# Kernel optimization log

Measured on AMD Instinct MI355X. Metric: run time of the kernel, lower is better.

The kernel has to match this reference:

```python
import jax, jax.numpy as jnp
import numpy as np
from jax import lax

N, H, W, T = 8, 100, 152, 256
STRIDE = 8
ANCHOR_SIZE = 64.0
PRE_NMS_THRESH = 0.05
PRE_NMS_TOP_N = 1000
NMS_THRESH = 0.6
POST_TOP_N = 100
IMG_H, IMG_W = 800, 1216
BW = (10.0, 10.0, 5.0, 5.0)          # BoxCoder weights (wx, wy, ww, wh)
DWH_CLIP = float(np.log(1000.0 / 16.0))
TO_REMOVE = 1.0


def setup_inputs() -> dict:
    key = jax.random.key(0)
    k1, k2, k3 = jax.random.split(key, 3)
    box_regression = jax.random.normal(k1, (N, 4, H, W), dtype=jnp.float32)
    centerness = jax.random.normal(k2, (N, 1, H, W), dtype=jnp.float32)
    dot_product_logits = jax.random.normal(k3, (N, H * W, T), dtype=jnp.float32)
    # anchor grid matching permute_and_flatten's (H, W, A) row-major ordering
    ys, xs = jnp.meshgrid(jnp.arange(H, dtype=jnp.float32),
                          jnp.arange(W, dtype=jnp.float32), indexing="ij")
    cx = xs.reshape(-1) * STRIDE + STRIDE / 2.0
    cy = ys.reshape(-1) * STRIDE + STRIDE / 2.0
    half = ANCHOR_SIZE / 2.0
    anc = jnp.stack([cx - half, cy - half, cx + half, cy + half], axis=-1)  # [H*W, 4]
    anchors = jnp.broadcast_to(anc, (N, H * W, 4)).astype(jnp.float32)
    return {"box_regression": box_regression, "centerness": centerness,
            "anchors": anchors, "dot_product_logits": dot_product_logits}


def _decode(rel, anc):
    w = anc[..., 2] - anc[..., 0] + TO_REMOVE
    h = anc[..., 3] - anc[..., 1] + TO_REMOVE
    cx = anc[..., 0] + 0.5 * w
    cy = anc[..., 1] + 0.5 * h
    dx = rel[..., 0] / BW[0]
    dy = rel[..., 1] / BW[1]
    dw = jnp.minimum(rel[..., 2] / BW[2], DWH_CLIP)
    dh = jnp.minimum(rel[..., 3] / BW[3], DWH_CLIP)
    pcx = dx * w + cx
    pcy = dy * h + cy
    pw = jnp.exp(dw) * w
    ph = jnp.exp(dh) * h
    return jnp.stack([pcx - 0.5 * pw, pcy - 0.5 * ph,
                      pcx + 0.5 * pw - 1.0, pcy + 0.5 * ph - 1.0], axis=-1)


def _iou_one_vs_all(box, boxes):
    area1 = (box[2] - box[0] + TO_REMOVE) * (box[3] - box[1] + TO_REMOVE)
    area2 = (boxes[:, 2] - boxes[:, 0] + TO_REMOVE) * (boxes[:, 3] - boxes[:, 1] + TO_REMOVE)
    lt = jnp.maximum(box[:2], boxes[:, :2])
    rb = jnp.minimum(box[2:], boxes[:, 2:])
    wh = jnp.maximum(rb - lt + TO_REMOVE, 0.0)
    inter = wh[:, 0] * wh[:, 1]
    return inter / (area1 + area2 - inter)


def _nms_single(boxes, scores):
    # greedy NMS, fixed POST_TOP_N iterations (fpn_post_nms_top_n)
    def step(s, _):
        j = jnp.argmax(s)
        sj = s[j]
        bj = boxes[j]
        flag = (sj > 0).astype(boxes.dtype)
        ious = _iou_one_vs_all(bj, boxes)
        s = jnp.where(ious > NMS_THRESH, 0.0, s).at[j].set(0.0)
        return s, (bj * flag, sj * flag)
    _, (kb, ks) = lax.scan(step, scores, None, length=POST_TOP_N)
    return kb, ks


def reference(box_regression, centerness, anchors, dot_product_logits):
    n, _, h, w = box_regression.shape
    # sigmoid + MEAN token aggregation  -> [N, HWA]
    scores = jax.nn.sigmoid(dot_product_logits).mean(-1)
    # permute_and_flatten: [N,4A,H,W] -> [N, HWA, 4]
    box_reg = box_regression.reshape(n, 1, 4, h, w).transpose(0, 3, 4, 1, 2).reshape(n, -1, 4)
    ctr = jax.nn.sigmoid(centerness.reshape(n, 1, 1, h, w).transpose(0, 3, 4, 1, 2).reshape(n, -1))
    cand = scores > PRE_NMS_THRESH          # threshold on raw aggregated scores
    cls = scores * ctr                      # centerness-weighted score
    masked = jnp.where(cand, cls, 0.0)
    vals, idx = lax.top_k(masked, PRE_NMS_TOP_N)          # per-image top-k candidates
    valid = jnp.take_along_axis(cand, idx, axis=1)        # [N, PRE_NMS_TOP_N]
    sel_reg = jnp.take_along_axis(box_reg, idx[..., None], axis=1)
    sel_anc = jnp.take_along_axis(anchors, idx[..., None], axis=1)
    boxes = _decode(sel_reg, sel_anc)
    # clip_to_image
    boxes = jnp.stack([
        jnp.clip(boxes[..., 0], 0.0, IMG_W - 1.0),
        jnp.clip(boxes[..., 1], 0.0, IMG_H - 1.0),
        jnp.clip(boxes[..., 2], 0.0, IMG_W - 1.0),
        jnp.clip(boxes[..., 3], 0.0, IMG_H - 1.0)], axis=-1)
    vf = valid.astype(boxes.dtype)
    det_scores = jnp.sqrt(jnp.where(valid, vals, 1.0)) * vf   # sqrt of cls*ctr, safe grad
    keep_boxes, keep_scores = jax.vmap(_nms_single)(boxes, det_scores)
    return keep_boxes, keep_scores
```

## Files before the change

kernel.cpp:

```cpp
#include <hip/hip_runtime.h>
#include <math.h>

#define NN 8
#define HH 100
#define WW 152
#define HW (HH*WW)
#define TT 256
#define TOPN 1000
#define CAP 1024
#define POSTN 100
#define NMS_T 0.6f
#define IMGW 1216
#define IMGH 800
#define DWH_CLIP 4.135166556742356f

typedef unsigned long long u64;
typedef unsigned int u32;

__global__ __launch_bounds__(256) void score_kernel(
    const float* __restrict__ logits,
    const float* __restrict__ centerness,
    float* __restrict__ masked)
{
    int wid  = blockIdx.x * 4 + (threadIdx.x >> 6);
    int lane = threadIdx.x & 63;
    const float4 v = *(reinterpret_cast<const float4*>(logits + (size_t)wid * TT) + lane);
    float s = 0.f;
    s += __fdividef(1.f, 1.f + expf(-v.x));
    s += __fdividef(1.f, 1.f + expf(-v.y));
    s += __fdividef(1.f, 1.f + expf(-v.z));
    s += __fdividef(1.f, 1.f + expf(-v.w));
    #pragma unroll
    for (int off = 32; off; off >>= 1) s += __shfl_xor(s, off, 64);
    if (lane == 0) {
        float score = s * (1.0f / 256.0f);
        float c = centerness[wid];
        float ctr = 1.f / (1.f + expf(-c));
        masked[wid] = (score > 0.05f) ? score * ctr : 0.f;
    }
}

__global__ __launch_bounds__(256) void select_nms_kernel(
    const float* __restrict__ masked,
    const float* __restrict__ box_reg,
    float* __restrict__ out)
{
    const int n    = blockIdx.x;
    const int tid  = threadIdx.x;
    const int wv   = tid >> 6;
    const int lane = tid & 63;
    const int PER  = (HW + 255) / 256;

    u32 bits[(HW + 255) / 256];
    const float* mb = masked + (size_t)n * HW;
    #pragma unroll
    for (int j = 0; j < PER; j++) {
        int e = tid + j * 256;
        bits[j] = (e < HW) ? __float_as_uint(mb[e]) : 0u;
    }

    __shared__ int    parts[2][4];
    __shared__ int    s_cnt1, s_cnt2, s_kept;
    __shared__ u64    keys[CAP];
    __shared__ float4 sbox[CAP];
    __shared__ float  sscr[CAP];

    float* outb = out + (size_t)n * POSTN * 4;
    float* outs = out + (size_t)NN * POSTN * 4 + (size_t)n * POSTN;

    int p = 0;
    u32 lo = 0u, hi = 0x3F800000u;
    while (lo < hi) {
        u32 mid = lo + ((hi - lo) >> 1);
        int c = 0;
        #pragma unroll
        for (int j = 0; j < PER; j++) c += (bits[j] > mid) ? 1 : 0;
        #pragma unroll
        for (int off = 32; off; off >>= 1) c += __shfl_xor(c, off, 64);
        if (lane == 0) parts[p][wv] = c;
        __syncthreads();
        int tot = parts[p][0] + parts[p][1] + parts[p][2] + parts[p][3];
        p ^= 1;
        if (tot <= TOPN - 1) hi = mid; else lo = mid + 1;
    }
    const u32 thr = lo;

    #pragma unroll
    for (int j = 0; j < CAP / 256; j++) keys[tid + j * 256] = 0ull;
    if (tid == 0) { s_cnt1 = 0; s_cnt2 = 0; }
    __syncthreads();
    #pragma unroll
    for (int j = 0; j < PER; j++) {
        int e = tid + j * 256;
        u32 v = bits[j];
        if (e < HW && v > thr) {
            int pos = atomicAdd(&s_cnt1, 1);
            if (pos < TOPN) keys[pos] = (((u64)v) << 32) | (u32)(~e);
        }
    }
    __syncthreads();
    const int c1 = min(s_cnt1, TOPN);
    if (thr > 0u) {
        #pragma unroll
        for (int j = 0; j < PER; j++) {
            int e = tid + j * 256;
            if (e < HW && bits[j] == thr) {
                int q = atomicAdd(&s_cnt2, 1);
                int pos = c1 + q;
                if (pos < TOPN) keys[pos] = (((u64)thr) << 32) | (u32)(~e);
            }
        }
    }
    __syncthreads();

    for (int k = 2; k <= CAP; k <<= 1) {
        for (int j2 = k >> 1; j2 > 0; j2 >>= 1) {
            #pragma unroll
            for (int e = 0; e < CAP / 256; e++) {
                int i = tid + e * 256;
                int ixj = i ^ j2;
                if (ixj > i) {
                    u64 a = keys[i], bb = keys[ixj];
                    bool sw = ((i & k) == 0) ? (a < bb) : (a > bb);
                    if (sw) { keys[i] = bb; keys[ixj] = a; }
                }
            }
            __syncthreads();
        }
    }

    #pragma unroll
    for (int e = 0; e < CAP / 256; e++) {
        int pos = tid + e * 256;
        u64 kk = keys[pos];
        float s = __uint_as_float((u32)(kk >> 32));
        float4 box = make_float4(0.f, 0.f, 0.f, 0.f);
        if (s > 0.f) {
            int loc = (int)(~(u32)kk);
            float acx = (float)(loc % WW) * 8.f + 4.f;
            float acy = (float)(loc / WW) * 8.f + 4.f;
            float a0 = acx - 32.f, a1 = acy - 32.f, a2 = acx + 32.f, a3 = acy + 32.f;
            float r0 = box_reg[((size_t)n * 4 + 0) * HW + loc];
            float r1 = box_reg[((size_t)n * 4 + 1) * HW + loc];
            float r2 = box_reg[((size_t)n * 4 + 2) * HW + loc];
            float r3 = box_reg[((size_t)n * 4 + 3) * HW + loc];
            float w  = a2 - a0 + 1.0f;
            float h  = a3 - a1 + 1.0f;
            float cx = a0 + 0.5f * w;
            float cy = a1 + 0.5f * h;
            float dx = r0 / 10.0f;
            float dy = r1 / 10.0f;
            float dw = fminf(r2 / 5.0f, DWH_CLIP);
            float dh = fminf(r3 / 5.0f, DWH_CLIP);
            float pcx = dx * w + cx;
            float pcy = dy * h + cy;
            float pw  = expf(dw) * w;
            float ph  = expf(dh) * h;
            float x1 = pcx - 0.5f * pw;
            float y1 = pcy - 0.5f * ph;
            float x2 = pcx + 0.5f * pw - 1.0f;
            float y2 = pcy + 0.5f * ph - 1.0f;
            box.x = fminf(fmaxf(x1, 0.f), (float)(IMGW - 1));
            box.y = fminf(fmaxf(y1, 0.f), (float)(IMGH - 1));
            box.z = fminf(fmaxf(x2, 0.f), (float)(IMGW - 1));
            box.w = fminf(fmaxf(y2, 0.f), (float)(IMGH - 1));
        }
        sbox[pos] = box;
        sscr[pos] = s;
    }
    __syncthreads();

    if (tid < 64) {
        float ax1 = 0.f, ay1 = 0.f, ax2 = 0.f, ay2 = 0.f, aar = 0.f;
        float bx1 = 0.f, by1 = 0.f, bx2 = 0.f, by2 = 0.f, bar = 0.f;
        int kept = 0;

        float  ns = sscr[0];
        float4 nb = sbox[0];
        for (int i = 0; i < CAP; ++i) {
            float  s  = ns;
            float4 cb = nb;
            int ip = i + 1;
            if (ip < CAP) { ns = sscr[ip]; nb = sbox[ip]; }
            if (s <= 0.f) break;

            float carea = (cb.z - cb.x + 1.f) * (cb.w - cb.y + 1.f);

            float ix1 = fmaxf(cb.x, ax1), iy1 = fmaxf(cb.y, ay1);
            float ix2 = fminf(cb.z, ax2), iy2 = fminf(cb.w, ay2);
            float iw = fmaxf(ix2 - ix1 + 1.f, 0.f), ih = fmaxf(iy2 - iy1 + 1.f, 0.f);
            float interA = iw * ih;
            float iouA = interA / (carea + aar - interA);

            ix1 = fmaxf(cb.x, bx1); iy1 = fmaxf(cb.y, by1);
            ix2 = fminf(cb.z, bx2); iy2 = fminf(cb.w, by2);
            iw = fmaxf(ix2 - ix1 + 1.f, 0.f); ih = fmaxf(iy2 - iy1 + 1.f, 0.f);
            float interB = iw * ih;
            float iouB = interB / (carea + bar - interB);

            bool supA = (tid < kept)      && (iouA > NMS_T);
            bool supB = (tid < kept - 64) && (iouB > NMS_T);
            u64 sup = __ballot(supA) | __ballot(supB);
            if (sup == 0ull) {
                if (kept < 64) {
                    if (tid == kept)      { ax1 = cb.x; ay1 = cb.y; ax2 = cb.z; ay2 = cb.w; aar = carea; }
                } else {
                    if (tid == kept - 64) { bx1 = cb.x; by1 = cb.y; bx2 = cb.z; by2 = cb.w; bar = carea; }
                }
                if (tid == 0) {
                    outb[kept * 4 + 0] = cb.x; outb[kept * 4 + 1] = cb.y;
                    outb[kept * 4 + 2] = cb.z; outb[kept * 4 + 3] = cb.w;
                    outs[kept] = sqrtf(s);
                }
                ++kept;
                if (kept == POSTN) break;
            }
        }
        if (tid == 0) s_kept = kept;
    }
    __syncthreads();

    const int cnt = s_kept;
    for (int i = cnt + tid; i < POSTN; i += 256) {
        outb[i * 4 + 0] = 0.f; outb[i * 4 + 1] = 0.f;
        outb[i * 4 + 2] = 0.f; outb[i * 4 + 3] = 0.f;
        outs[i] = 0.f;
    }
}

extern "C" void kernel_launch(void* const* d_in, const int* in_sizes, int n_in,
                              void* d_out, int out_size, void* d_ws, size_t ws_size,
                              hipStream_t stream) {
    const float* box_reg = (const float*)d_in[0];
    const float* center  = (const float*)d_in[1];
    const float* logits  = (const float*)d_in[3];
    float* out = (float*)d_out;

    float* masked = (float*)d_ws;

    score_kernel<<<(NN * HW) / 4, 256, 0, stream>>>(logits, center, masked);
    select_nms_kernel<<<NN, 256, 0, stream>>>(masked, box_reg, out);
}
```

Before: 283.5 us.

## Stage scores in LDS, exit threshold search early, and batch NMS in chunks of eight

The per-image score array is now staged in shared memory with vectorized uint4 loads, replacing the per-thread register array. The binary search for the top-k threshold stops as soon as the candidate count falls between TOPN and CAP, which removes later iterations and the tie pass. Keys beyond TOPN are zeroed after the sort. The serial NMS loop now handles 8 candidates per step: IoU against the kept boxes is computed for all 8, pairwise suppression inside the group comes from one ballot, and the IoU division is replaced by a double-precision multiply compare. This cuts per-candidate ballots and serial latency, but the early exit could select a different candidate set and the double compare adds FP64 work.

Measured after the change: 283.4 us. About the same (-0.1%).

```diff
diff --git a/kernel.cpp b/kernel.cpp
--- a/kernel.cpp
+++ b/kernel.cpp
@@ -5,11 +5,11 @@
 #define HH 100
 #define WW 152
 #define HW (HH*WW)
+#define HWP 15360
 #define TT 256
 #define TOPN 1000
 #define CAP 1024
 #define POSTN 100
-#define NMS_T 0.6f
 #define IMGW 1216
 #define IMGH 800
 #define DWH_CLIP 4.135166556742356f
@@ -40,7 +40,7 @@
     }
 }
 
-__global__ __launch_bounds__(256) void select_nms_kernel(
+__global__ __launch_bounds__(256, 1) void select_nms_kernel(
     const float* __restrict__ masked,
     const float* __restrict__ box_reg,
     float* __restrict__ out)
@@ -49,69 +49,88 @@
     const int tid  = threadIdx.x;
     const int wv   = tid >> 6;
     const int lane = tid & 63;
-    const int PER  = (HW + 255) / 256;
-
-    u32 bits[(HW + 255) / 256];
-    const float* mb = masked + (size_t)n * HW;
-    #pragma unroll
-    for (int j = 0; j < PER; j++) {
-        int e = tid + j * 256;
-        bits[j] = (e < HW) ? __float_as_uint(mb[e]) : 0u;
-    }
-
-    __shared__ int    parts[2][4];
-    __shared__ int    s_cnt1, s_cnt2, s_kept;
+
+    __shared__ __align__(16) u32 lbits[HWP];
     __shared__ u64    keys[CAP];
     __shared__ float4 sbox[CAP];
     __shared__ float  sscr[CAP];
+    __shared__ int    parts[2][4];
+    __shared__ int    s_cnt1, s_cnt2, s_kept;
 
     float* outb = out + (size_t)n * POSTN * 4;
     float* outs = out + (size_t)NN * POSTN * 4 + (size_t)n * POSTN;
 
+    {
+        const uint4* mb4 = reinterpret_cast<const uint4*>(masked + (size_t)n * HW);
+        uint4* lb4 = reinterpret_cast<uint4*>(lbits);
+        #pragma unroll
+        for (int j = 0; j < HWP / 1024; j++) {
+            int f = j * 256 + tid;
+            uint4 v = make_uint4(0u, 0u, 0u, 0u);
+            if (f < HW / 4) v = mb4[f];
+            lb4[f] = v;
+        }
+    }
+    __syncthreads();
+
     int p = 0;
     u32 lo = 0u, hi = 0x3F800000u;
+    u32 thr = 0u;
+    bool early = false;
     while (lo < hi) {
         u32 mid = lo + ((hi - lo) >> 1);
         int c = 0;
-        #pragma unroll
-        for (int j = 0; j < PER; j++) c += (bits[j] > mid) ? 1 : 0;
+        const uint4* lb4 = reinterpret_cast<const uint4*>(lbits);
+        #pragma unroll
+        for (int j = 0; j < HWP / 1024; j++) {
+            uint4 v = lb4[j * 256 + tid];
+            c += (v.x > mid) + (v.y > mid) + (v.z > mid) + (v.w > mid);
+        }
         #pragma unroll
         for (int off = 32; off; off >>= 1) c += __shfl_xor(c, off, 64);
         if (lane == 0) parts[p][wv] = c;
         __syncthreads();
         int tot = parts[p][0] + parts[p][1] + parts[p][2] + parts[p][3];
         p ^= 1;
+        if (tot >= TOPN && tot <= CAP) { thr = mid; early = true; break; }
         if (tot <= TOPN - 1) hi = mid; else lo = mid + 1;
     }
-    const u32 thr = lo;
+    if (!early) thr = lo;
 
     #pragma unroll
     for (int j = 0; j < CAP / 256; j++) keys[tid + j * 256] = 0ull;
     if (tid == 0) { s_cnt1 = 0; s_cnt2 = 0; }
     __syncthreads();
-    #pragma unroll
-    for (int j = 0; j < PER; j++) {
-        int e = tid + j * 256;
-        u32 v = bits[j];
-        if (e < HW && v > thr) {
-            int pos = atomicAdd(&s_cnt1, 1);
-            if (pos < TOPN) keys[pos] = (((u64)v) << 32) | (u32)(~e);
-        }
-    }
-    __syncthreads();
-    const int c1 = min(s_cnt1, TOPN);
-    if (thr > 0u) {
-        #pragma unroll
-        for (int j = 0; j < PER; j++) {
-            int e = tid + j * 256;
-            if (e < HW && bits[j] == thr) {
-                int q = atomicAdd(&s_cnt2, 1);
-                int pos = c1 + q;
-                if (pos < TOPN) keys[pos] = (((u64)thr) << 32) | (u32)(~e);
-            }
-        }
-    }
-    __syncthreads();
+    {
+        const uint4* lb4 = reinterpret_cast<const uint4*>(lbits);
+        #pragma unroll
+        for (int j = 0; j < HWP / 1024; j++) {
+            int f = j * 256 + tid;
+            uint4 v = lb4[f];
+            int e = f * 4;
+            if (v.x > thr) { int q = atomicAdd(&s_cnt1, 1); if (q < CAP) keys[q] = (((u64)v.x) << 32) | (u32)(~(e + 0)); }
+            if (v.y > thr) { int q = atomicAdd(&s_cnt1, 1); if (q < CAP) keys[q] = (((u64)v.y) << 32) | (u32)(~(e + 1)); }
+            if (v.z > thr) { int q = atomicAdd(&s_cnt1, 1); if (q < CAP) keys[q] = (((u64)v.z) << 32) | (u32)(~(e + 2)); }
+            if (v.w > thr) { int q = atomicAdd(&s_cnt1, 1); if (q < CAP) keys[q] = (((u64)v.w) << 32) | (u32)(~(e + 3)); }
+        }
+    }
+    __syncthreads();
+    if (!early && thr > 0u) {
+        const int c1 = min(s_cnt1, TOPN);
+        const uint4* lb4 = reinterpret_cast<const uint4*>(lbits);
+        #pragma unroll
+        for (int j = 0; j < HWP / 1024; j++) {
+            int f = j * 256 + tid;
+            uint4 v = lb4[f];
+            int e = f * 4;
+            if (v.x == thr) { int q = atomicAdd(&s_cnt2, 1); if (c1 + q < TOPN) keys[c1 + q] = (((u64)thr) << 32) | (u32)(~(e + 0)); }
+            if (v.y == thr) { int q = atomicAdd(&s_cnt2, 1); if (c1 + q < TOPN) keys[c1 + q] = (((u64)thr) << 32) | (u32)(~(e + 1)); }
+            if (v.z == thr) { int q = atomicAdd(&s_cnt2, 1); if (c1 + q < TOPN) keys[c1 + q] = (((u64)thr) << 32) | (u32)(~(e + 2)); }
+            if (v.w == thr) { int q = atomicAdd(&s_cnt2, 1); if (c1 + q < TOPN) keys[c1 + q] = (((u64)thr) << 32) | (u32)(~(e + 3)); }
+        }
+        __syncthreads();
+    }
+    if (early) __syncthreads();
 
     for (int k = 2; k <= CAP; k <<= 1) {
         for (int j2 = k >> 1; j2 > 0; j2 >>= 1) {
@@ -128,6 +147,8 @@
             __syncthreads();
         }
     }
+    if (tid < CAP - TOPN) keys[TOPN + tid] = 0ull;
+    __syncthreads();
 
     #pragma unroll
     for (int e = 0; e < CAP / 256; e++) {
@@ -173,50 +194,81 @@
     if (tid < 64) {
         float ax1 = 0.f, ay1 = 0.f, ax2 = 0.f, ay2 = 0.f, aar = 0.f;
         float bx1 = 0.f, by1 = 0.f, bx2 = 0.f, by2 = 0.f, bar = 0.f;
-        int kept = 0;
-
-        float  ns = sscr[0];
-        float4 nb = sbox[0];
-        for (int i = 0; i < CAP; ++i) {
-            float  s  = ns;
-            float4 cb = nb;
-            int ip = i + 1;
-            if (ip < CAP) { ns = sscr[ip]; nb = sbox[ip]; }
-            if (s <= 0.f) break;
-
-            float carea = (cb.z - cb.x + 1.f) * (cb.w - cb.y + 1.f);
-
-            float ix1 = fmaxf(cb.x, ax1), iy1 = fmaxf(cb.y, ay1);
-            float ix2 = fminf(cb.z, ax2), iy2 = fminf(cb.w, ay2);
-            float iw = fmaxf(ix2 - ix1 + 1.f, 0.f), ih = fmaxf(iy2 - iy1 + 1.f, 0.f);
-            float interA = iw * ih;
-            float iouA = interA / (carea + aar - interA);
-
-            ix1 = fmaxf(cb.x, bx1); iy1 = fmaxf(cb.y, by1);
-            ix2 = fminf(cb.z, bx2); iy2 = fminf(cb.w, by2);
-            iw = fmaxf(ix2 - ix1 + 1.f, 0.f); ih = fmaxf(iy2 - iy1 + 1.f, 0.f);
-            float interB = iw * ih;
-            float iouB = interB / (carea + bar - interB);
-
-            bool supA = (tid < kept)      && (iouA > NMS_T);
-            bool supB = (tid < kept - 64) && (iouB > NMS_T);
-            u64 sup = __ballot(supA) | __ballot(supB);
-            if (sup == 0ull) {
-                if (kept < 64) {
-                    if (tid == kept)      { ax1 = cb.x; ay1 = cb.y; ax2 = cb.z; ay2 = cb.w; aar = carea; }
-                } else {
-                    if (tid == kept - 64) { bx1 = cb.x; by1 = cb.y; bx2 = cb.z; by2 = cb.w; bar = carea; }
+        int  kept = 0;
+        bool done = false;
+        const double MD = (double)0.6f + 0x1p-25;
+        const int pa = lane >> 3, pb = lane & 7;
+
+        for (int i0 = 0; i0 < CAP && !done; i0 += 8) {
+            u32 myMask = 0u, dMask = 0u;
+            #pragma unroll
+            for (int c = 0; c < 8; c++) {
+                float  s  = sscr[i0 + c];
+                float4 cb = sbox[i0 + c];
+                if (s <= 0.f) dMask |= (1u << c);
+                float carea = (cb.z - cb.x + 1.f) * (cb.w - cb.y + 1.f);
+
+                float ix1 = fmaxf(cb.x, ax1), iy1 = fmaxf(cb.y, ay1);
+                float ix2 = fminf(cb.z, ax2), iy2 = fminf(cb.w, ay2);
+                float iw = fmaxf(ix2 - ix1 + 1.f, 0.f), ih = fmaxf(iy2 - iy1 + 1.f, 0.f);
+                float interA = iw * ih;
+                float denomA = (carea + aar) - interA;
+                bool supA = (lane < kept) && ((double)interA > MD * (double)denomA);
+
+                ix1 = fmaxf(cb.x, bx1); iy1 = fmaxf(cb.y, by1);
+                ix2 = fminf(cb.z, bx2); iy2 = fminf(cb.w, by2);
+                iw = fmaxf(ix2 - ix1 + 1.f, 0.f); ih = fmaxf(iy2 - iy1 + 1.f, 0.f);
+                float interB = iw * ih;
+                float denomB = (carea + bar) - interB;
+                bool supB = (lane < kept - 64) && ((double)interB > MD * (double)denomB);
+
+                if (supA || supB) myMask |= (1u << c);
+            }
+            #pragma unroll
+            for (int off = 32; off; off >>= 1) myMask |= __shfl_xor(myMask, off, 64);
+
+            bool psup = false;
+            if (pa < pb) {
+                float4 A = sbox[i0 + pa];
+                float4 B = sbox[i0 + pb];
+                float areaA = (A.z - A.x + 1.f) * (A.w - A.y + 1.f);
+                float areaB = (B.z - B.x + 1.f) * (B.w - B.y + 1.f);
+                float ix1 = fmaxf(A.x, B.x), iy1 = fmaxf(A.y, B.y);
+                float ix2 = fminf(A.z, B.z), iy2 = fminf(A.w, B.w);
+                float iw = fmaxf(ix2 - ix1 + 1.f, 0.f), ih = fmaxf(iy2 - iy1 + 1.f, 0.f);
+                float inter = iw * ih;
+                float denom = (areaA + areaB) - inter;
+                psup = ((double)inter > MD * (double)denom);
+            }
+            u64 P = __ballot(psup);
+
+            u64 kbytes = 0ull;
+            for (int c = 0; c < 8; c++) {
+                if ((dMask >> c) & 1u) { done = true; break; }
+                u32 sup = (myMask >> c) & 1u;
+                u64 col = (P >> c) & 0x0101010101010101ull;
+                if (col & kbytes) sup = 1u;
+                if (!sup) {
+                    float4 cb = sbox[i0 + c];
+                    float  s  = sscr[i0 + c];
+                    float carea = (cb.z - cb.x + 1.f) * (cb.w - cb.y + 1.f);
+                    if (kept < 64) {
+                        if (lane == kept)      { ax1 = cb.x; ay1 = cb.y; ax2 = cb.z; ay2 = cb.w; aar = carea; }
+                    } else {
+                        if (lane == kept - 64) { bx1 = cb.x; by1 = cb.y; bx2 = cb.z; by2 = cb.w; bar = carea; }
+                    }
+                    if (lane == 0) {
+                        outb[kept * 4 + 0] = cb.x; outb[kept * 4 + 1] = cb.y;
+                        outb[kept * 4 + 2] = cb.z; outb[kept * 4 + 3] = cb.w;
+                        outs[kept] = sqrtf(s);
+                    }
+                    kbytes |= 1ull << (8 * c);
+                    ++kept;
+                    if (kept == POSTN) { done = true; break; }
                 }
-                if (tid == 0) {
-                    outb[kept * 4 + 0] = cb.x; outb[kept * 4 + 1] = cb.y;
-                    outb[kept * 4 + 2] = cb.z; outb[kept * 4 + 3] = cb.w;
-                    outs[kept] = sqrtf(s);
-                }
-                ++kept;
-                if (kept == POSTN) break;
-            }
-        }
-        if (tid == 0) s_kept = kept;
+            }
+        }
+        if (lane == 0) s_kept = kept;
     }
     __syncthreads();
 
```
